# Optimization experiments

Hardware: AMD Instinct MI355X
Metric: run time of the kernel (lower is better)

Reference implementation:

```python
import jax, jax.numpy as jnp
import numpy as np

B, S, D, H = 2, 2048, 1024, 16
DK = D // H  # 64


def setup_inputs() -> dict:
    key = jax.random.key(0)
    ks = jax.random.split(key, 5)
    std = 0.02
    return {
        "x": jax.random.normal(ks[0], (B, S, D), dtype=jnp.float32),
        "Wq": jax.random.normal(ks[1], (D, D), dtype=jnp.float32) * std,
        "bq": jnp.zeros((D,), jnp.float32),
        "Wk": jax.random.normal(ks[2], (D, D), dtype=jnp.float32) * std,
        "bk": jnp.zeros((D,), jnp.float32),
        "Wv": jax.random.normal(ks[3], (D, D), dtype=jnp.float32) * std,
        "bv": jnp.zeros((D,), jnp.float32),
        "Wo": jax.random.normal(ks[4], (D, D), dtype=jnp.float32) * std,
        "bo": jnp.zeros((D,), jnp.float32),
    }


def reference(x, Wq, bq, Wk, bk, Wv, bv, Wo, bo):
    b, s, d = x.shape
    # QKV projections (torch Linear: x @ W.T + b)
    q = x @ Wq.T + bq
    k = x @ Wk.T + bk
    v = x @ Wv.T + bv
    # [b, s, d] -> [b, h, s, d_k]
    q = q.reshape(b, s, H, DK).transpose(0, 2, 1, 3)
    k = k.reshape(b, s, H, DK).transpose(0, 2, 1, 3)
    v = v.reshape(b, s, H, DK).transpose(0, 2, 1, 3)
    # scaled dot-product scores [b, h, s, s]
    scores = jnp.einsum('bhqd,bhkd->bhqk', q, k) / np.float32(np.sqrt(DK))
    # causal mask (mask=True path in original forward)
    causal = jnp.tril(jnp.ones((s, s), dtype=bool))
    scores = jnp.where(causal, scores, jnp.float32(-1e9))
    attn = jax.nn.softmax(scores, axis=-1)
    # dropout is identity in eval / p=0
    out = jnp.einsum('bhqk,bhkd->bhqd', attn, v)
    out = out.transpose(0, 2, 1, 3).reshape(b, s, d)
    return out @ Wo.T + bo
```

## Files before the change

### kernel.cpp

```cpp
#include <hip/hip_runtime.h>
#include <stdint.h>
#include <math.h>

#define B_ 2
#define S_ 2048
#define D_ 1024
#define H_ 16
#define DK_ 64
#define M_ (B_*S_)
#define NT_ 16

typedef unsigned short u16;
typedef unsigned int u32;
typedef __attribute__((ext_vector_type(8))) __bf16 bf16x8;
typedef __attribute__((ext_vector_type(4))) float f32x4;

#define AS1 __attribute__((address_space(1)))
#define AS3 __attribute__((address_space(3)))

__device__ __forceinline__ u16 f2bf(float f) {
  u32 u = __float_as_uint(f);
  return (u16)((u + 0x7fffu + ((u >> 16) & 1u)) >> 16);
}
__device__ __forceinline__ u16 f2bfr(float f) {
  return (u16)((__float_as_uint(f) + 0x8000u) >> 16);
}

__device__ __forceinline__ void gload_lds16(const void* g, void* lds) {
  __builtin_amdgcn_global_load_lds((const AS1 u32*)g,
                                   (AS3 u32*)(u32)(uintptr_t)lds, 16, 0, 0);
}

__device__ __forceinline__ f32x4 mfma16(bf16x8 a, bf16x8 b, f32x4 c) {
  return __builtin_amdgcn_mfma_f32_16x16x32_bf16(a, b, c, 0, 0, 0);
}

#define VMCNT_(n) asm volatile("s_waitcnt vmcnt(" #n ")" ::: "memory")
#define VMCNT(n) VMCNT_(n)

__global__ __launch_bounds__(256) void f2bf_kernel(const float* __restrict__ in,
                                                   u16* __restrict__ out, int n4) {
  int i = blockIdx.x * 256 + threadIdx.x;
  if (i >= n4) return;
  float4 v = ((const float4*)in)[i];
  u32 lo = (u32)f2bf(v.x) | ((u32)f2bf(v.y) << 16);
  u32 hi = (u32)f2bf(v.z) | ((u32)f2bf(v.w) << 16);
  ((uint2*)out)[i] = make_uint2(lo, hi);
}

__global__ __launch_bounds__(256) void f2bf4_kernel(
    const float* __restrict__ W0, const float* __restrict__ W1,
    const float* __restrict__ W2, const float* __restrict__ W3,
    u16* __restrict__ o0, u16* __restrict__ o1, u16* __restrict__ o2, u16* __restrict__ o3,
    int n4) {
  const float* src; u16* dst;
  switch (blockIdx.y) {
    case 0: src = W0; dst = o0; break;
    case 1: src = W1; dst = o1; break;
    case 2: src = W2; dst = o2; break;
    default: src = W3; dst = o3; break;
  }
  int i = blockIdx.x * 256 + threadIdx.x;
  if (i >= n4) return;
  float4 v = ((const float4*)src)[i];
  u32 lo = (u32)f2bf(v.x) | ((u32)f2bf(v.y) << 16);
  u32 hi = (u32)f2bf(v.z) | ((u32)f2bf(v.w) << 16);
  ((uint2*)dst)[i] = make_uint2(lo, hi);
}

__global__ __launch_bounds__(512, 2) void gemm_qkv_8ph(
    const u16* __restrict__ A,
    const u16* __restrict__ W0, const u16* __restrict__ W1, const u16* __restrict__ W2,
    const float* __restrict__ b0, const float* __restrict__ b1, const float* __restrict__ b2,
    u16* __restrict__ C0, u16* __restrict__ C1, u16* __restrict__ C2) {
  const int id = blockIdx.x;
  const int xcd = id & 7, k = id >> 3;
  const int my = xcd*2 + (k & 1);
  const int rest = k >> 1;
  const int z = rest >> 2, nx = rest & 3;

  const u16* W = (z == 0) ? W0 : (z == 1) ? W1 : W2;
  const float* bias = (z == 0) ? b0 : (z == 1) ? b1 : b2;
  u16* C = (z == 0) ? C0 : (z == 1) ? C1 : C2;
  const float osc = (z == 0) ? 0.18033688f : 1.0f;
  const int mbase = my*256, nbase = nx*256;

  __shared__ u16 LA[2][256*64];
  __shared__ u16 LB[2][256*64];

  const int tid = threadIdx.x;
  const int w = tid >> 6, lane = tid & 63;
  const int lo = lane & 15, hi = lane >> 4;
  const int wr = w >> 2, wc = w & 3;

  const int sr = tid >> 3;
  const int sc = tid & 7;
  const int sx = (sc ^ (sr & 7)) * 8;

#define STAGE_A(buf, t, h) do {                                                   \
    int gr_ = sr + (h)*64;                                                        \
    size_t g_ = (size_t)(mbase + gr_)*D_ + (size_t)(t)*64 + sx;                   \
    gload_lds16(&A[g_],            &LA[buf][gr_*64 + sc*8]);                      \
    gload_lds16(&A[g_ + 128*D_],   &LA[buf][(gr_ + 128)*64 + sc*8]);              \
  } while (0)

#define STAGE_B(buf, t, h) do {                                                   \
    int gr_ = (sr & 31) + (h)*32 + (sr >> 5)*64;                                  \
    size_t g_ = (size_t)(nbase + gr_)*D_ + (size_t)(t)*64 + sx;                   \
    gload_lds16(&W[g_],            &LB[buf][gr_*64 + sc*8]);                      \
    gload_lds16(&W[g_ + 128*D_],   &LB[buf][(gr_ + 128)*64 + sc*8]);              \
  } while (0)

#define LDA_F(dst, buf, mq, kk) do {                                              \
    _Pragma("unroll")                                                             \
    for (int m_ = 0; m_ < 4; ++m_) {                                              \
      int R_ = wr*128 + (mq)*64 + m_*16 + lo;                                     \
      dst[m_] = *(const bf16x8*)&LA[buf][R_*64 + ((((kk)*4 + hi) ^ (R_ & 7))*8)]; \
    }                                                                             \
  } while (0)

#define LDB_F(dst, buf, kk) do {                                                  \
    _Pragma("unroll")                                                             \
    for (int q_ = 0; q_ < 2; ++q_)                                                \
      _Pragma("unroll")                                                           \
      for (int n_ = 0; n_ < 2; ++n_) {                                            \
        int R_ = wc*64 + q_*32 + n_*16 + lo;                                      \
        dst[q_][n_] =                                                             \
            *(const bf16x8*)&LB[buf][R_*64 + ((((kk)*4 + hi) ^ (R_ & 7))*8)];     \
      }                                                                           \
  } while (0)

#define MM(mq, af_, bv_) do {                                                     \
    __builtin_amdgcn_s_setprio(1);                                                \
    _Pragma("unroll")                                                             \
    for (int m_ = 0; m_ < 4; ++m_)                                                \
      _Pragma("unroll")                                                           \
      for (int q_ = 0; q_ < 2; ++q_)                                              \
        _Pragma("unroll")                                                         \
        for (int n_ = 0; n_ < 2; ++n_)                                            \
          acc[(mq)*4 + m_][q_*2 + n_] =                                           \
              mfma16(bv_[q_][n_], af_[m_], acc[(mq)*4 + m_][q_*2 + n_]);          \
    __builtin_amdgcn_s_setprio(0);                                                \
  } while (0)

#define BAR __builtin_amdgcn_s_barrier()

  f32x4 acc[8][4] = {};

#define TILE(buf, t) do {                                                         \
    const int tn1_ = ((t) + 1 < NT_) ? (t) + 1 : NT_ - 1;                         \
    const int tn2_ = ((t) + 2 < NT_) ? (t) + 2 : NT_ - 1;                         \
    bf16x8 af[4], bv0[2][2], bv1[2][2];                                           \
                                                              \
    LDA_F(af, buf, 0, 0); LDB_F(bv0, buf, 0);                                     \
    STAGE_B(1 - (buf), tn1_, 1);                                                  \
    BAR; MM(0, af, bv0); BAR;                                                     \
                                                              \
    LDA_F(af, buf, 0, 1); LDB_F(bv1, buf, 1);                                     \
    STAGE_A(1 - (buf), tn1_, 1);                                                  \
    VMCNT(8);                                                                     \
    BAR; MM(0, af, bv1); BAR;                                                     \
                                                 \
    LDA_F(af, buf, 1, 0);                                                         \
    STAGE_A(buf, tn2_, 0);                                                        \
    BAR; MM(1, af, bv0); BAR;                                                     \
                                                 \
    LDA_F(af, buf, 1, 1);                                                         \
    STAGE_B(buf, tn2_, 0);                                                        \
    VMCNT(6);                                                                     \
    BAR; MM(1, af, bv1); BAR;                                                     \
  } while (0)

  STAGE_A(0, 0, 0); STAGE_B(0, 0, 0);
  STAGE_B(0, 0, 1); STAGE_A(0, 0, 1);
  STAGE_A(1, 1, 0); STAGE_B(1, 1, 0);
  VMCNT(6);
  BAR;

  for (int j = 0; j < NT_/2; ++j) {
    TILE(0, 2*j);
    TILE(1, 2*j + 1);
  }

#pragma unroll
  for (int m = 0; m < 8; ++m) {
    int row = mbase + wr*128 + m*16 + lo;
#pragma unroll
    for (int n = 0; n < 4; ++n) {
      int colb = nbase + wc*64 + n*16 + hi*4;
      float4 b4 = *(const float4*)&bias[colb];
      u32 d01 = (u32)f2bf((acc[m][n][0] + b4.x) * osc)
              | ((u32)f2bf((acc[m][n][1] + b4.y) * osc) << 16);
      u32 d23 = (u32)f2bf((acc[m][n][2] + b4.z) * osc)
              | ((u32)f2bf((acc[m][n][3] + b4.w) * osc) << 16);
      *(uint2*)&C[(size_t)row*D_ + colb] = make_uint2(d01, d23);
    }
  }
#undef TILE
#undef MM
#undef LDA_F
#undef LDB_F
#undef STAGE_A
#undef STAGE_B
#undef BAR
}

__global__ __launch_bounds__(256) void gemm_bt64(
    const u16* __restrict__ A, const u16* __restrict__ W,
    const float* __restrict__ bias, float* __restrict__ C,
    int M, int N, int K) {
  __shared__ u16 As[64*32];
  __shared__ u16 Bs[128*32];
  const int tid = threadIdx.x;
  const int wave = tid >> 6, lane = tid & 63;
  const int lo = lane & 15, hi = lane >> 4;
  const int mbase = blockIdx.y * 64, nbase = blockIdx.x * 128;

  f32x4 acc[4][2] = {};

  for (int k0 = 0; k0 < K; k0 += 32) {
    {
      int row = tid >> 2;
      int col = (tid & 3) * 8;
      gload_lds16(&A[(size_t)(mbase + row)*K + k0 + col], &As[row*32 + col]);
#pragma unroll
      for (int i = 0; i < 2; ++i)
        gload_lds16(&W[(size_t)(nbase + i*64 + row)*K + k0 + col], &Bs[(i*64 + row)*32 + col]);
    }
    __syncthreads();
    bf16x8 af[4], bfr[2];
#pragma unroll
    for (int m = 0; m < 4; ++m)
      af[m] = *(const bf16x8*)&As[(m*16 + lo)*32 + hi*8];
#pragma unroll
    for (int n = 0; n < 2; ++n)
      bfr[n] = *(const bf16x8*)&Bs[(wave*32 + n*16 + lo)*32 + hi*8];
#pragma unroll
    for (int m = 0; m < 4; ++m)
#pragma unroll
      for (int n = 0; n < 2; ++n)
        acc[m][n] = mfma16(bfr[n], af[m], acc[m][n]);
    __syncthreads();
  }

#pragma unroll
  for (int m = 0; m < 4; ++m) {
    int row = mbase + m*16 + lo;
#pragma unroll
    for (int n = 0; n < 2; ++n) {
      int colb = nbase + wave*32 + n*16 + hi*4;
      float4 b4 = *(const float4*)&bias[colb];
      float4 ov = make_float4(acc[m][n][0] + b4.x, acc[m][n][1] + b4.y,
                              acc[m][n][2] + b4.z, acc[m][n][3] + b4.w);
      *(float4*)&C[(size_t)row*N + colb] = ov;
    }
  }
}

__global__ __launch_bounds__(256) void transpose_v(const u16* __restrict__ V,
                                                   u16* __restrict__ Vt) {
  const int st = blockIdx.x, bh = blockIdx.y;
  const int b = bh >> 4, h = bh & 15;
  __shared__ u16 tile[64][72];
  const int tid = threadIdx.x;
#pragma unroll
  for (int c = 0; c < 2; ++c) {
    int s = c*32 + (tid >> 3);
    int d0 = (tid & 7) * 8;
    *(uint4*)&tile[s][d0] =
        *(const uint4*)&V[((size_t)(b*S_ + st*64 + s))*D_ + h*DK_ + d0];
  }
  __syncthreads();
#pragma unroll
  for (int c = 0; c < 2; ++c) {
    int d = c*32 + (tid >> 3);
    int s0 = (tid & 7) * 8;
    uint4 ov;
    u16* tp = (u16*)&ov;
#pragma unroll
    for (int jj = 0; jj < 8; ++jj) tp[jj] = tile[s0 + jj][d];
    *(uint4*)&Vt[((size_t)(bh*DK_ + d))*S_ + st*64 + s0] = ov;
  }
}

__global__ __launch_bounds__(256) void attn_kernel(
    const u16* __restrict__ Q, const u16* __restrict__ K, const u16* __restrict__ Vt,
    u16* __restrict__ AO) {
  const int blk = blockIdx.x;
  const int xcd = blk & 7, slot = blk >> 3;
  const int bh = xcd + 8*(slot & 3);
  const int qt = 31 - (slot >> 2);
  const int b = bh >> 4, h = bh & 15;
  const int tid = threadIdx.x, w = tid >> 6, lane = tid & 63;
  const int lo = lane & 15, hi = lane >> 4;

  __shared__ u16 Kl[2][64*64];
  __shared__ u16 Vl[2][64*64];
  __shared__ u16 Pl[4][16*72];

  const int r8 = lane >> 3;
  const int rloc = w*8 + r8;
  const int xorcol = ((lane & 7) ^ r8) * 8;
  const size_t kbase = (size_t)b*S_*D_ + (size_t)h*DK_;
  const size_t vbase = (size_t)bh*DK_*S_;
  const size_t koff0 = kbase + (size_t)rloc*D_ + xorcol;
  const size_t koff1 = kbase + (size_t)(32 + rloc)*D_ + xorcol;
  const size_t voff0 = vbase + (size_t)rloc*S_ + xorcol;
  const size_t voff1 = vbase + (size_t)(32 + rloc)*S_ + xorcol;
  const int ldsoff = rloc*64 + (lane & 7)*8;

  const int qrow = qt*64 + w*16 + lo;
  bf16x8 qf[2];
#pragma unroll
  for (int kk = 0; kk < 2; ++kk)
    qf[kk] = *(const bf16x8*)&Q[(size_t)(b*S_ + qrow)*D_ + h*DK_ + kk*32 + hi*8];

  f32x4 o[4] = {};
  float mr = -INFINITY, lr = 0.f;

  gload_lds16(&K[koff0], &Kl[0][ldsoff]);
  gload_lds16(&K[koff1], &Kl[0][2048 + ldsoff]);
  gload_lds16(&Vt[voff0], &Vl[0][ldsoff]);
  gload_lds16(&Vt[voff1], &Vl[0][2048 + ldsoff]);

  for (int kt = 0; kt <= qt; ++kt) {
    const int cur = kt & 1;
    __syncthreads();
    if (kt < qt) {
      const size_t kadd = (size_t)(kt + 1)*64*D_;
      const int vadd = (kt + 1)*64;
      gload_lds16(&K[koff0 + kadd], &Kl[cur ^ 1][ldsoff]);
      gload_lds16(&K[koff1 + kadd], &Kl[cur ^ 1][2048 + ldsoff]);
      gload_lds16(&Vt[voff0 + vadd], &Vl[cur ^ 1][ldsoff]);
      gload_lds16(&Vt[voff1 + vadd], &Vl[cur ^ 1][2048 + ldsoff]);
    }

    f32x4 s[4] = {};
#pragma unroll
    for (int kk = 0; kk < 2; ++kk) {
#pragma unroll
      for (int n = 0; n < 4; ++n) {
        int row = n*16 + lo;
        bf16x8 kf = *(const bf16x8*)&Kl[cur][row*64 + (((kk*4 + hi) ^ (row & 7)) * 8)];
        s[n] = __builtin_amdgcn_mfma_f32_16x16x32_bf16(kf, qf[kk], s[n], 0, 0, 0);
      }
    }

    if (kt == qt) {
      const int ql = w*16 + lo;
#pragma unroll
      for (int n = 0; n < 4; ++n)
#pragma unroll
        for (int j = 0; j < 4; ++j)
          if (n*16 + hi*4 + j > ql) s[n][j] = -INFINITY;
    }

    float pm = -INFINITY;
#pragma unroll
    for (int n = 0; n < 4; ++n)
#pragma unroll
      for (int j = 0; j < 4; ++j) pm = fmaxf(pm, s[n][j]);

    if (!__all(pm <= mr + 11.0f)) {
      pm = fmaxf(pm, __shfl_xor(pm, 16));
      pm = fmaxf(pm, __shfl_xor(pm, 32));
      float mn = fmaxf(mr, pm);
      float corr = __builtin_amdgcn_exp2f(mr - mn);
      mr = mn;
      lr *= corr;
#pragma unroll
      for (int n = 0; n < 4; ++n)
#pragma unroll
        for (int j = 0; j < 4; ++j) o[n][j] *= corr;
    }

#pragma unroll
    for (int n = 0; n < 4; ++n) {
      float p0 = __builtin_amdgcn_exp2f(s[n][0] - mr);
      float p1 = __builtin_amdgcn_exp2f(s[n][1] - mr);
      float p2 = __builtin_amdgcn_exp2f(s[n][2] - mr);
      float p3 = __builtin_amdgcn_exp2f(s[n][3] - mr);
      lr += (p0 + p1) + (p2 + p3);
      u32 d01 = (u32)f2bfr(p0) | ((u32)f2bfr(p1) << 16);
      u32 d23 = (u32)f2bfr(p2) | ((u32)f2bfr(p3) << 16);
      *(uint2*)&Pl[w][lo*72 + n*16 + hi*4] = make_uint2(d01, d23);
    }

#pragma unroll
    for (int kk = 0; kk < 2; ++kk) {
      bf16x8 pf = *(const bf16x8*)&Pl[w][lo*72 + kk*32 + hi*8];
#pragma unroll
      for (int n = 0; n < 4; ++n) {
        int row = n*16 + lo;
        bf16x8 vf = *(const bf16x8*)&Vl[cur][row*64 + (((kk*4 + hi) ^ (row & 7)) * 8)];
        o[n] = __builtin_amdgcn_mfma_f32_16x16x32_bf16(vf, pf, o[n], 0, 0, 0);
      }
    }
  }

  lr += __shfl_xor(lr, 16);
  lr += __shfl_xor(lr, 32);
  const float rinv = __builtin_amdgcn_rcpf(lr);
  const size_t obase = (size_t)(b*S_ + qrow)*D_ + h*DK_;
#pragma unroll
  for (int n = 0; n < 4; ++n) {
    u32 d01 = (u32)f2bf(o[n][0] * rinv) | ((u32)f2bf(o[n][1] * rinv) << 16);
    u32 d23 = (u32)f2bf(o[n][2] * rinv) | ((u32)f2bf(o[n][3] * rinv) << 16);
    *(uint2*)&AO[obase + n*16 + hi*4] = make_uint2(d01, d23);
  }
}

extern "C" void kernel_launch(void* const* d_in, const int* in_sizes, int n_in,
                              void* d_out, int out_size, void* d_ws, size_t ws_size,
                              hipStream_t stream) {
  const float* x  = (const float*)d_in[0];
  const float* Wq = (const float*)d_in[1];
  const float* bq = (const float*)d_in[2];
  const float* Wk = (const float*)d_in[3];
  const float* bk = (const float*)d_in[4];
  const float* Wv = (const float*)d_in[5];
  const float* bv = (const float*)d_in[6];
  const float* Wo = (const float*)d_in[7];
  const float* bo = (const float*)d_in[8];

  char* ws = (char*)d_ws;
  const size_t MB = 1048576;
  u16* xb  = (u16*)(ws + 0);
  u16* Wqb = (u16*)(ws + 8*MB);
  u16* Wkb = (u16*)(ws + 10*MB);
  u16* Wvb = (u16*)(ws + 12*MB);
  u16* Wob = (u16*)(ws + 14*MB);
  u16* Qb  = (u16*)(ws + 16*MB);
  u16* Kb  = (u16*)(ws + 24*MB);
  u16* Vb  = (u16*)(ws + 32*MB);
  u16* Vtb = (u16*)(ws + 0);
  u16* AOb = (u16*)(ws + 32*MB);

  f2bf_kernel<<<4096, 256, 0, stream>>>(x, xb, (M_*D_)/4);
  f2bf4_kernel<<<dim3(1024, 4), 256, 0, stream>>>(Wq, Wk, Wv, Wo,
                                                  Wqb, Wkb, Wvb, Wob, (D_*D_)/4);

  gemm_qkv_8ph<<<192, 512, 0, stream>>>(xb, Wqb, Wkb, Wvb, bq, bk, bv, Qb, Kb, Vb);

  transpose_v<<<dim3(32, 32), 256, 0, stream>>>(Vb, Vtb);

  attn_kernel<<<1024, 256, 0, stream>>>(Qb, Kb, Vtb, AOb);

  gemm_bt64<<<dim3(8, 64), 256, 0, stream>>>(AOb, Wob, bo, (float*)d_out, M_, D_, D_);
}
```

Before: 115.1 us.

## Fuse V transpose into QKV GEMM epilogue and double query rows per attention block

The QKV GEMM now swaps MFMA operand order for the V projection and writes V directly in transposed [b, feature, s] layout, which removes the separate transpose_v kernel and its round trip through global memory. The attention kernel now handles 128 query rows per block (32 per wave, in two 16-row groups), so each loaded K/V tile serves twice as many queries, and the grid is halved. Waves skip tiles that lie entirely beyond their causal limit. The cost is more registers per wave and a less balanced causal workload, and the transposed V stores are narrower and strided.

```diff
diff --git a/kernel.cpp b/kernel.cpp
--- a/kernel.cpp
+++ b/kernel.cpp
@@ -83,6 +83,7 @@
   const float* bias = (z == 0) ? b0 : (z == 1) ? b1 : b2;
   u16* C = (z == 0) ? C0 : (z == 1) ? C1 : C2;
   const float osc = (z == 0) ? 0.18033688f : 1.0f;
+  const bool vz = (z == 2);
   const int mbase = my*256, nbase = nx*256;
 
   __shared__ u16 LA[2][256*64];
@@ -132,14 +133,25 @@
 
 #define MM(mq, af_, bv_) do {                                                     \
     __builtin_amdgcn_s_setprio(1);                                                \
-    _Pragma("unroll")                                                             \
-    for (int m_ = 0; m_ < 4; ++m_)                                                \
+    if (vz) {                                                                     \
       _Pragma("unroll")                                                           \
-      for (int q_ = 0; q_ < 2; ++q_)                                              \
+      for (int m_ = 0; m_ < 4; ++m_)                                              \
         _Pragma("unroll")                                                         \
-        for (int n_ = 0; n_ < 2; ++n_)                                            \
-          acc[(mq)*4 + m_][q_*2 + n_] =                                           \
-              mfma16(bv_[q_][n_], af_[m_], acc[(mq)*4 + m_][q_*2 + n_]);          \
+        for (int q_ = 0; q_ < 2; ++q_)                                            \
+          _Pragma("unroll")                                                       \
+          for (int n_ = 0; n_ < 2; ++n_)                                          \
+            acc[(mq)*4 + m_][q_*2 + n_] =                                         \
+                mfma16(af_[m_], bv_[q_][n_], acc[(mq)*4 + m_][q_*2 + n_]);        \
+    } else {                                                                      \
+      _Pragma("unroll")                                                           \
+      for (int m_ = 0; m_ < 4; ++m_)                                              \
+        _Pragma("unroll")                                                         \
+        for (int q_ = 0; q_ < 2; ++q_)                                            \
+          _Pragma("unroll")                                                       \
+          for (int n_ = 0; n_ < 2; ++n_)                                          \
+            acc[(mq)*4 + m_][q_*2 + n_] =                                         \
+                mfma16(bv_[q_][n_], af_[m_], acc[(mq)*4 + m_][q_*2 + n_]);        \
+    }                                                                             \
     __builtin_amdgcn_s_setprio(0);                                                \
   } while (0)
 
@@ -182,18 +194,36 @@
     TILE(1, 2*j + 1);
   }
 
-#pragma unroll
-  for (int m = 0; m < 8; ++m) {
-    int row = mbase + wr*128 + m*16 + lo;
-#pragma unroll
-    for (int n = 0; n < 4; ++n) {
-      int colb = nbase + wc*64 + n*16 + hi*4;
-      float4 b4 = *(const float4*)&bias[colb];
-      u32 d01 = (u32)f2bf((acc[m][n][0] + b4.x) * osc)
-              | ((u32)f2bf((acc[m][n][1] + b4.y) * osc) << 16);
-      u32 d23 = (u32)f2bf((acc[m][n][2] + b4.z) * osc)
-              | ((u32)f2bf((acc[m][n][3] + b4.w) * osc) << 16);
-      *(uint2*)&C[(size_t)row*D_ + colb] = make_uint2(d01, d23);
+  if (!vz) {
+#pragma unroll
+    for (int m = 0; m < 8; ++m) {
+      int row = mbase + wr*128 + m*16 + lo;
+#pragma unroll
+      for (int n = 0; n < 4; ++n) {
+        int colb = nbase + wc*64 + n*16 + hi*4;
+        float4 b4 = *(const float4*)&bias[colb];
+        u32 d01 = (u32)f2bf((acc[m][n][0] + b4.x) * osc)
+                | ((u32)f2bf((acc[m][n][1] + b4.y) * osc) << 16);
+        u32 d23 = (u32)f2bf((acc[m][n][2] + b4.z) * osc)
+                | ((u32)f2bf((acc[m][n][3] + b4.w) * osc) << 16);
+        *(uint2*)&C[(size_t)row*D_ + colb] = make_uint2(d01, d23);
+      }
+    }
+  } else {
+#pragma unroll
+    for (int m = 0; m < 8; ++m) {
+      int s0 = mbase + wr*128 + m*16 + hi*4;
+      int bb = s0 >> 11, sl = s0 & (S_ - 1);
+#pragma unroll
+      for (int n = 0; n < 4; ++n) {
+        int feat = nbase + wc*64 + n*16 + lo;
+        float bvv = bias[feat];
+        u32 d01 = (u32)f2bf(acc[m][n][0] + bvv)
+                | ((u32)f2bf(acc[m][n][1] + bvv) << 16);
+        u32 d23 = (u32)f2bf(acc[m][n][2] + bvv)
+                | ((u32)f2bf(acc[m][n][3] + bvv) << 16);
+        *(uint2*)&C[((size_t)(bb*1024 + feat))*S_ + sl] = make_uint2(d01, d23);
+      }
     }
   }
 #undef TILE
@@ -257,46 +287,21 @@
   }
 }
 
-__global__ __launch_bounds__(256) void transpose_v(const u16* __restrict__ V,
-                                                   u16* __restrict__ Vt) {
-  const int st = blockIdx.x, bh = blockIdx.y;
-  const int b = bh >> 4, h = bh & 15;
-  __shared__ u16 tile[64][72];
-  const int tid = threadIdx.x;
-#pragma unroll
-  for (int c = 0; c < 2; ++c) {
-    int s = c*32 + (tid >> 3);
-    int d0 = (tid & 7) * 8;
-    *(uint4*)&tile[s][d0] =
-        *(const uint4*)&V[((size_t)(b*S_ + st*64 + s))*D_ + h*DK_ + d0];
-  }
-  __syncthreads();
-#pragma unroll
-  for (int c = 0; c < 2; ++c) {
-    int d = c*32 + (tid >> 3);
-    int s0 = (tid & 7) * 8;
-    uint4 ov;
-    u16* tp = (u16*)&ov;
-#pragma unroll
-    for (int jj = 0; jj < 8; ++jj) tp[jj] = tile[s0 + jj][d];
-    *(uint4*)&Vt[((size_t)(bh*DK_ + d))*S_ + st*64 + s0] = ov;
-  }
-}
-
 __global__ __launch_bounds__(256) void attn_kernel(
     const u16* __restrict__ Q, const u16* __restrict__ K, const u16* __restrict__ Vt,
     u16* __restrict__ AO) {
   const int blk = blockIdx.x;
   const int xcd = blk & 7, slot = blk >> 3;
   const int bh = xcd + 8*(slot & 3);
-  const int qt = 31 - (slot >> 2);
+  const int qt = 15 - (slot >> 2);
   const int b = bh >> 4, h = bh & 15;
   const int tid = threadIdx.x, w = tid >> 6, lane = tid & 63;
   const int lo = lane & 15, hi = lane >> 4;
+  const int nkt = 2*qt + 2;
 
   __shared__ u16 Kl[2][64*64];
   __shared__ u16 Vl[2][64*64];
-  __shared__ u16 Pl[4][16*72];
+  __shared__ u16 Pl[4][32*72];
 
   const int r8 = lane >> 3;
   const int rloc = w*8 + r8;
@@ -309,24 +314,30 @@
   const size_t voff1 = vbase + (size_t)(32 + rloc)*S_ + xorcol;
   const int ldsoff = rloc*64 + (lane & 7)*8;
 
-  const int qrow = qt*64 + w*16 + lo;
-  bf16x8 qf[2];
-#pragma unroll
-  for (int kk = 0; kk < 2; ++kk)
-    qf[kk] = *(const bf16x8*)&Q[(size_t)(b*S_ + qrow)*D_ + h*DK_ + kk*32 + hi*8];
-
-  f32x4 o[4] = {};
-  float mr = -INFINITY, lr = 0.f;
+  int qr[2];
+  bf16x8 qf[2][2];
+#pragma unroll
+  for (int g = 0; g < 2; ++g) {
+    qr[g] = qt*128 + w*32 + g*16 + lo;
+#pragma unroll
+    for (int kk = 0; kk < 2; ++kk)
+      qf[g][kk] = *(const bf16x8*)&Q[(size_t)(b*S_ + qr[g])*D_ + h*DK_ + kk*32 + hi*8];
+  }
+
+  f32x4 o[2][4] = {};
+  float mr[2] = {-INFINITY, -INFINITY}, lr[2] = {0.f, 0.f};
 
   gload_lds16(&K[koff0], &Kl[0][ldsoff]);
   gload_lds16(&K[koff1], &Kl[0][2048 + ldsoff]);
   gload_lds16(&Vt[voff0], &Vl[0][ldsoff]);
   gload_lds16(&Vt[voff1], &Vl[0][2048 + ldsoff]);
 
-  for (int kt = 0; kt <= qt; ++kt) {
+  const int wave_qmax = qt*128 + w*32 + 31;
+
+  for (int kt = 0; kt < nkt; ++kt) {
     const int cur = kt & 1;
     __syncthreads();
-    if (kt < qt) {
+    if (kt + 1 < nkt) {
       const size_t kadd = (size_t)(kt + 1)*64*D_;
       const int vadd = (kt + 1)*64;
       gload_lds16(&K[koff0 + kadd], &Kl[cur ^ 1][ldsoff]);
@@ -335,78 +346,94 @@
       gload_lds16(&Vt[voff1 + vadd], &Vl[cur ^ 1][2048 + ldsoff]);
     }
 
-    f32x4 s[4] = {};
+    if (kt*64 > wave_qmax) continue;
+
+    f32x4 s[2][4] = {};
 #pragma unroll
     for (int kk = 0; kk < 2; ++kk) {
 #pragma unroll
       for (int n = 0; n < 4; ++n) {
         int row = n*16 + lo;
         bf16x8 kf = *(const bf16x8*)&Kl[cur][row*64 + (((kk*4 + hi) ^ (row & 7)) * 8)];
-        s[n] = __builtin_amdgcn_mfma_f32_16x16x32_bf16(kf, qf[kk], s[n], 0, 0, 0);
-      }
-    }
-
-    if (kt == qt) {
-      const int ql = w*16 + lo;
+        s[0][n] = mfma16(kf, qf[0][kk], s[0][n]);
+        s[1][n] = mfma16(kf, qf[1][kk], s[1][n]);
+      }
+    }
+
+    if (kt >= 2*qt) {
+#pragma unroll
+      for (int g = 0; g < 2; ++g)
+#pragma unroll
+        for (int n = 0; n < 4; ++n)
+#pragma unroll
+          for (int j = 0; j < 4; ++j)
+            if (kt*64 + n*16 + hi*4 + j > qr[g]) s[g][n][j] = -INFINITY;
+    }
+
+    float pm[2] = {-INFINITY, -INFINITY};
+#pragma unroll
+    for (int g = 0; g < 2; ++g)
 #pragma unroll
       for (int n = 0; n < 4; ++n)
 #pragma unroll
-        for (int j = 0; j < 4; ++j)
-          if (n*16 + hi*4 + j > ql) s[n][j] = -INFINITY;
-    }
-
-    float pm = -INFINITY;
-#pragma unroll
-    for (int n = 0; n < 4; ++n)
-#pragma unroll
-      for (int j = 0; j < 4; ++j) pm = fmaxf(pm, s[n][j]);
-
-    if (!__all(pm <= mr + 11.0f)) {
-      pm = fmaxf(pm, __shfl_xor(pm, 16));
-      pm = fmaxf(pm, __shfl_xor(pm, 32));
-      float mn = fmaxf(mr, pm);
-      float corr = __builtin_amdgcn_exp2f(mr - mn);
-      mr = mn;
-      lr *= corr;
-#pragma unroll
-      for (int n = 0; n < 4; ++n)
-#pragma unroll
-        for (int j = 0; j < 4; ++j) o[n][j] *= corr;
-    }
-
-#pragma unroll
-    for (int n = 0; n < 4; ++n) {
-      float p0 = __builtin_amdgcn_exp2f(s[n][0] - mr);
-      float p1 = __builtin_amdgcn_exp2f(s[n][1] - mr);
-      float p2 = __builtin_amdgcn_exp2f(s[n][2] - mr);
-      float p3 = __builtin_amdgcn_exp2f(s[n][3] - mr);
-      lr += (p0 + p1) + (p2 + p3);
-      u32 d01 = (u32)f2bfr(p0) | ((u32)f2bfr(p1) << 16);
-      u32 d23 = (u32)f2bfr(p2) | ((u32)f2bfr(p3) << 16);
-      *(uint2*)&Pl[w][lo*72 + n*16 + hi*4] = make_uint2(d01, d23);
-    }
+        for (int j = 0; j < 4; ++j) pm[g] = fmaxf(pm[g], s[g][n][j]);
+
+    if (!__all(fmaxf(pm[0] - mr[0], pm[1] - mr[1]) <= 11.0f)) {
+#pragma unroll
+      for (int g = 0; g < 2; ++g) {
+        float t = fmaxf(pm[g], __shfl_xor(pm[g], 16));
+        t = fmaxf(t, __shfl_xor(t, 32));
+        float mn = fmaxf(mr[g], t);
+        float corr = __builtin_amdgcn_exp2f(mr[g] - mn);
+        mr[g] = mn;
+        lr[g] *= corr;
+#pragma unroll
+        for (int n = 0; n < 4; ++n)
+#pragma unroll
+          for (int j = 0; j < 4; ++j) o[g][n][j] *= corr;
+      }
+    }
+
+#pragma unroll
+    for (int g = 0; g < 2; ++g)
+#pragma unroll
+      for (int n = 0; n < 4; ++n) {
+        float p0 = __builtin_amdgcn_exp2f(s[g][n][0] - mr[g]);
+        float p1 = __builtin_amdgcn_exp2f(s[g][n][1] - mr[g]);
+        float p2 = __builtin_amdgcn_exp2f(s[g][n][2] - mr[g]);
+        float p3 = __builtin_amdgcn_exp2f(s[g][n][3] - mr[g]);
+        lr[g] += (p0 + p1) + (p2 + p3);
+        u32 d01 = (u32)f2bfr(p0) | ((u32)f2bfr(p1) << 16);
+        u32 d23 = (u32)f2bfr(p2) | ((u32)f2bfr(p3) << 16);
+        *(uint2*)&Pl[w][(g*16 + lo)*72 + n*16 + hi*4] = make_uint2(d01, d23);
+      }
 
 #pragma unroll
     for (int kk = 0; kk < 2; ++kk) {
-      bf16x8 pf = *(const bf16x8*)&Pl[w][lo*72 + kk*32 + hi*8];
+      bf16x8 pf0 = *(const bf16x8*)&Pl[w][lo*72 + kk*32 + hi*8];
+      bf16x8 pf1 = *(const bf16x8*)&Pl[w][(16 + lo)*72 + kk*32 + hi*8];
 #pragma unroll
       for (int n = 0; n < 4; ++n) {
         int row = n*16 + lo;
         bf16x8 vf = *(const bf16x8*)&Vl[cur][row*64 + (((kk*4 + hi) ^ (row & 7)) * 8)];
-        o[n] = __builtin_amdgcn_mfma_f32_16x16x32_bf16(vf, pf, o[n], 0, 0, 0);
-      }
-    }
-  }
-
-  lr += __shfl_xor(lr, 16);
-  lr += __shfl_xor(lr, 32);
-  const float rinv = __builtin_amdgcn_rcpf(lr);
-  const size_t obase = (size_t)(b*S_ + qrow)*D_ + h*DK_;
-#pragma unroll
-  for (int n = 0; n < 4; ++n) {
-    u32 d01 = (u32)f2bf(o[n][0] * rinv) | ((u32)f2bf(o[n][1] * rinv) << 16);
-    u32 d23 = (u32)f2bf(o[n][2] * rinv) | ((u32)f2bf(o[n][3] * rinv) << 16);
-    *(uint2*)&AO[obase + n*16 + hi*4] = make_uint2(d01, d23);
+        o[0][n] = mfma16(vf, pf0, o[0][n]);
+        o[1][n] = mfma16(vf, pf1, o[1][n]);
+      }
+    }
+  }
+
+#pragma unroll
+  for (int g = 0; g < 2; ++g) {
+    lr[g] += __shfl_xor(lr[g], 16);
+    lr[g] += __shfl_xor(lr[g], 32);
+    const float rinv = __builtin_amdgcn_rcpf(lr[g]);
+    const size_t obase = (size_t)(b*S_ + qr[g])*D_ + h*DK_;
+#pragma unroll
+    for (int n = 0; n < 4; ++n) {
+      u32 d01 = (u32)f2bf(o[g][n][0] * rinv) | ((u32)f2bf(o[g][n][1] * rinv) << 16);
+      u32 d23 = (u32)f2bf(o[g][n][2] * rinv) | ((u32)f2bf(o[g][n][3] * rinv) << 16);
+      *(uint2*)&AO[obase + n*16 + hi*4] = make_uint2(d01, d23);
+    }
   }
 }
 
@@ -432,19 +459,16 @@
   u16* Wob = (u16*)(ws + 14*MB);
   u16* Qb  = (u16*)(ws + 16*MB);
   u16* Kb  = (u16*)(ws + 24*MB);
-  u16* Vb  = (u16*)(ws + 32*MB);
-  u16* Vtb = (u16*)(ws + 0);
-  u16* AOb = (u16*)(ws + 32*MB);
+  u16* Vtb = (u16*)(ws + 32*MB);
+  u16* AOb = (u16*)(ws + 0);
 
   f2bf_kernel<<<4096, 256, 0, stream>>>(x, xb, (M_*D_)/4);
   f2bf4_kernel<<<dim3(1024, 4), 256, 0, stream>>>(Wq, Wk, Wv, Wo,
                                                   Wqb, Wkb, Wvb, Wob, (D_*D_)/4);
 
-  gemm_qkv_8ph<<<192, 512, 0, stream>>>(xb, Wqb, Wkb, Wvb, bq, bk, bv, Qb, Kb, Vb);
-
-  transpose_v<<<dim3(32, 32), 256, 0, stream>>>(Vb, Vtb);
-
-  attn_kernel<<<1024, 256, 0, stream>>>(Qb, Kb, Vtb, AOb);
+  gemm_qkv_8ph<<<192, 512, 0, stream>>>(xb, Wqb, Wkb, Wvb, bq, bk, bv, Qb, Kb, Vtb);
+
+  attn_kernel<<<512, 256, 0, stream>>>(Qb, Kb, Vtb, AOb);
 
   gemm_bt64<<<dim3(8, 64), 256, 0, stream>>>(AOb, Wob, bo, (float*)d_out, M_, D_, D_);
 }
```

Result: slower. 131.0 us (+13.9%).

## Fuse V transpose into QKV GEMM epilogue and use packed bf16 conversion

Applied to the files above, without the earlier changes.

For the V projection, the QKV GEMM swaps the MFMA operand order so each lane holds consecutive sequence positions. It then writes V directly in the transposed [b,h,d,s] layout, which removes the separate transpose_v kernel and its extra read and write of V. Bf16 packing in the GEMM epilogue and in the attention kernel now uses the hardware v_cvt_pk_bf16_f32 instruction instead of manual integer rounding. This adds a branch on the z slice inside the MFMA macro, and the transposed stores write only 8 bytes of contiguous data per lane.

```diff
diff --git a/kernel.cpp b/kernel.cpp
--- a/kernel.cpp
+++ b/kernel.cpp
@@ -22,8 +22,11 @@
   u32 u = __float_as_uint(f);
   return (u16)((u + 0x7fffu + ((u >> 16) & 1u)) >> 16);
 }
-__device__ __forceinline__ u16 f2bfr(float f) {
-  return (u16)((__float_as_uint(f) + 0x8000u) >> 16);
+
+__device__ __forceinline__ u32 cvtpk(float a, float b) {
+  u32 r;
+  asm("v_cvt_pk_bf16_f32 %0, %1, %2" : "=v"(r) : "v"(a), "v"(b));
+  return r;
 }
 
 __device__ __forceinline__ void gload_lds16(const void* g, void* lds) {
@@ -43,9 +46,8 @@
   int i = blockIdx.x * 256 + threadIdx.x;
   if (i >= n4) return;
   float4 v = ((const float4*)in)[i];
-  u32 lo = (u32)f2bf(v.x) | ((u32)f2bf(v.y) << 16);
-  u32 hi = (u32)f2bf(v.z) | ((u32)f2bf(v.w) << 16);
-  ((uint2*)out)[i] = make_uint2(lo, hi);
+  ((uint2*)out)[i] = make_uint2((u32)f2bf(v.x) | ((u32)f2bf(v.y) << 16),
+                                (u32)f2bf(v.z) | ((u32)f2bf(v.w) << 16));
 }
 
 __global__ __launch_bounds__(256) void f2bf4_kernel(
@@ -63,9 +65,8 @@
   int i = blockIdx.x * 256 + threadIdx.x;
   if (i >= n4) return;
   float4 v = ((const float4*)src)[i];
-  u32 lo = (u32)f2bf(v.x) | ((u32)f2bf(v.y) << 16);
-  u32 hi = (u32)f2bf(v.z) | ((u32)f2bf(v.w) << 16);
-  ((uint2*)dst)[i] = make_uint2(lo, hi);
+  ((uint2*)dst)[i] = make_uint2((u32)f2bf(v.x) | ((u32)f2bf(v.y) << 16),
+                                (u32)f2bf(v.z) | ((u32)f2bf(v.w) << 16));
 }
 
 __global__ __launch_bounds__(512, 2) void gemm_qkv_8ph(
@@ -83,6 +84,7 @@
   const float* bias = (z == 0) ? b0 : (z == 1) ? b1 : b2;
   u16* C = (z == 0) ? C0 : (z == 1) ? C1 : C2;
   const float osc = (z == 0) ? 0.18033688f : 1.0f;
+  const bool vz = (z == 2);
   const int mbase = my*256, nbase = nx*256;
 
   __shared__ u16 LA[2][256*64];
@@ -132,14 +134,25 @@
 
 #define MM(mq, af_, bv_) do {                                                     \
     __builtin_amdgcn_s_setprio(1);                                                \
-    _Pragma("unroll")                                                             \
-    for (int m_ = 0; m_ < 4; ++m_)                                                \
+    if (vz) {                                                                     \
       _Pragma("unroll")                                                           \
-      for (int q_ = 0; q_ < 2; ++q_)                                              \
+      for (int m_ = 0; m_ < 4; ++m_)                                              \
         _Pragma("unroll")                                                         \
-        for (int n_ = 0; n_ < 2; ++n_)                                            \
-          acc[(mq)*4 + m_][q_*2 + n_] =                                           \
-              mfma16(bv_[q_][n_], af_[m_], acc[(mq)*4 + m_][q_*2 + n_]);          \
+        for (int q_ = 0; q_ < 2; ++q_)                                            \
+          _Pragma("unroll")                                                       \
+          for (int n_ = 0; n_ < 2; ++n_)                                          \
+            acc[(mq)*4 + m_][q_*2 + n_] =                                         \
+                mfma16(af_[m_], bv_[q_][n_], acc[(mq)*4 + m_][q_*2 + n_]);        \
+    } else {                                                                      \
+      _Pragma("unroll")                                                           \
+      for (int m_ = 0; m_ < 4; ++m_)                                              \
+        _Pragma("unroll")                                                         \
+        for (int q_ = 0; q_ < 2; ++q_)                                            \
+          _Pragma("unroll")                                                       \
+          for (int n_ = 0; n_ < 2; ++n_)                                          \
+            acc[(mq)*4 + m_][q_*2 + n_] =                                         \
+                mfma16(bv_[q_][n_], af_[m_], acc[(mq)*4 + m_][q_*2 + n_]);        \
+    }                                                                             \
     __builtin_amdgcn_s_setprio(0);                                                \
   } while (0)
 
@@ -151,20 +164,16 @@
     const int tn1_ = ((t) + 1 < NT_) ? (t) + 1 : NT_ - 1;                         \
     const int tn2_ = ((t) + 2 < NT_) ? (t) + 2 : NT_ - 1;                         \
     bf16x8 af[4], bv0[2][2], bv1[2][2];                                           \
-                                                              \
     LDA_F(af, buf, 0, 0); LDB_F(bv0, buf, 0);                                     \
     STAGE_B(1 - (buf), tn1_, 1);                                                  \
     BAR; MM(0, af, bv0); BAR;                                                     \
-                                                              \
     LDA_F(af, buf, 0, 1); LDB_F(bv1, buf, 1);                                     \
     STAGE_A(1 - (buf), tn1_, 1);                                                  \
     VMCNT(8);                                                                     \
     BAR; MM(0, af, bv1); BAR;                                                     \
-                                                 \
     LDA_F(af, buf, 1, 0);                                                         \
     STAGE_A(buf, tn2_, 0);                                                        \
     BAR; MM(1, af, bv0); BAR;                                                     \
-                                                 \
     LDA_F(af, buf, 1, 1);                                                         \
     STAGE_B(buf, tn2_, 0);                                                        \
     VMCNT(6);                                                                     \
@@ -182,18 +191,32 @@
     TILE(1, 2*j + 1);
   }
 
-#pragma unroll
-  for (int m = 0; m < 8; ++m) {
-    int row = mbase + wr*128 + m*16 + lo;
-#pragma unroll
-    for (int n = 0; n < 4; ++n) {
-      int colb = nbase + wc*64 + n*16 + hi*4;
-      float4 b4 = *(const float4*)&bias[colb];
-      u32 d01 = (u32)f2bf((acc[m][n][0] + b4.x) * osc)
-              | ((u32)f2bf((acc[m][n][1] + b4.y) * osc) << 16);
-      u32 d23 = (u32)f2bf((acc[m][n][2] + b4.z) * osc)
-              | ((u32)f2bf((acc[m][n][3] + b4.w) * osc) << 16);
-      *(uint2*)&C[(size_t)row*D_ + colb] = make_uint2(d01, d23);
+  if (!vz) {
+#pragma unroll
+    for (int m = 0; m < 8; ++m) {
+      int row = mbase + wr*128 + m*16 + lo;
+#pragma unroll
+      for (int n = 0; n < 4; ++n) {
+        int colb = nbase + wc*64 + n*16 + hi*4;
+        float4 b4 = *(const float4*)&bias[colb];
+        *(uint2*)&C[(size_t)row*D_ + colb] = make_uint2(
+            cvtpk((acc[m][n][0] + b4.x) * osc, (acc[m][n][1] + b4.y) * osc),
+            cvtpk((acc[m][n][2] + b4.z) * osc, (acc[m][n][3] + b4.w) * osc));
+      }
+    }
+  } else {
+#pragma unroll
+    for (int m = 0; m < 8; ++m) {
+      int s0 = mbase + wr*128 + m*16 + hi*4;
+      int bb = s0 >> 11, sl = s0 & (S_ - 1);
+#pragma unroll
+      for (int n = 0; n < 4; ++n) {
+        int feat = nbase + wc*64 + n*16 + lo;
+        float bvv = bias[feat];
+        *(uint2*)&C[((size_t)(bb*1024 + feat))*S_ + sl] = make_uint2(
+            cvtpk(acc[m][n][0] + bvv, acc[m][n][1] + bvv),
+            cvtpk(acc[m][n][2] + bvv, acc[m][n][3] + bvv));
+      }
     }
   }
 #undef TILE
@@ -257,32 +280,6 @@
   }
 }
 
-__global__ __launch_bounds__(256) void transpose_v(const u16* __restrict__ V,
-                                                   u16* __restrict__ Vt) {
-  const int st = blockIdx.x, bh = blockIdx.y;
-  const int b = bh >> 4, h = bh & 15;
-  __shared__ u16 tile[64][72];
-  const int tid = threadIdx.x;
-#pragma unroll
-  for (int c = 0; c < 2; ++c) {
-    int s = c*32 + (tid >> 3);
-    int d0 = (tid & 7) * 8;
-    *(uint4*)&tile[s][d0] =
-        *(const uint4*)&V[((size_t)(b*S_ + st*64 + s))*D_ + h*DK_ + d0];
-  }
-  __syncthreads();
-#pragma unroll
-  for (int c = 0; c < 2; ++c) {
-    int d = c*32 + (tid >> 3);
-    int s0 = (tid & 7) * 8;
-    uint4 ov;
-    u16* tp = (u16*)&ov;
-#pragma unroll
-    for (int jj = 0; jj < 8; ++jj) tp[jj] = tile[s0 + jj][d];
-    *(uint4*)&Vt[((size_t)(bh*DK_ + d))*S_ + st*64 + s0] = ov;
-  }
-}
-
 __global__ __launch_bounds__(256) void attn_kernel(
     const u16* __restrict__ Q, const u16* __restrict__ K, const u16* __restrict__ Vt,
     u16* __restrict__ AO) {
@@ -342,7 +339,7 @@
       for (int n = 0; n < 4; ++n) {
         int row = n*16 + lo;
         bf16x8 kf = *(const bf16x8*)&Kl[cur][row*64 + (((kk*4 + hi) ^ (row & 7)) * 8)];
-        s[n] = __builtin_amdgcn_mfma_f32_16x16x32_bf16(kf, qf[kk], s[n], 0, 0, 0);
+        s[n] = mfma16(kf, qf[kk], s[n]);
       }
     }
 
@@ -381,9 +378,8 @@
       float p2 = __builtin_amdgcn_exp2f(s[n][2] - mr);
       float p3 = __builtin_amdgcn_exp2f(s[n][3] - mr);
       lr += (p0 + p1) + (p2 + p3);
-      u32 d01 = (u32)f2bfr(p0) | ((u32)f2bfr(p1) << 16);
-      u32 d23 = (u32)f2bfr(p2) | ((u32)f2bfr(p3) << 16);
-      *(uint2*)&Pl[w][lo*72 + n*16 + hi*4] = make_uint2(d01, d23);
+      *(uint2*)&Pl[w][lo*72 + n*16 + hi*4] =
+          make_uint2(cvtpk(p0, p1), cvtpk(p2, p3));
     }
 
 #pragma unroll
@@ -393,7 +389,7 @@
       for (int n = 0; n < 4; ++n) {
         int row = n*16 + lo;
         bf16x8 vf = *(const bf16x8*)&Vl[cur][row*64 + (((kk*4 + hi) ^ (row & 7)) * 8)];
-        o[n] = __builtin_amdgcn_mfma_f32_16x16x32_bf16(vf, pf, o[n], 0, 0, 0);
+        o[n] = mfma16(vf, pf, o[n]);
       }
     }
   }
@@ -404,9 +400,9 @@
   const size_t obase = (size_t)(b*S_ + qrow)*D_ + h*DK_;
 #pragma unroll
   for (int n = 0; n < 4; ++n) {
-    u32 d01 = (u32)f2bf(o[n][0] * rinv) | ((u32)f2bf(o[n][1] * rinv) << 16);
-    u32 d23 = (u32)f2bf(o[n][2] * rinv) | ((u32)f2bf(o[n][3] * rinv) << 16);
-    *(uint2*)&AO[obase + n*16 + hi*4] = make_uint2(d01, d23);
+    *(uint2*)&AO[obase + n*16 + hi*4] =
+        make_uint2(cvtpk(o[n][0] * rinv, o[n][1] * rinv),
+                   cvtpk(o[n][2] * rinv, o[n][3] * rinv));
   }
 }
 
@@ -432,17 +428,14 @@
   u16* Wob = (u16*)(ws + 14*MB);
   u16* Qb  = (u16*)(ws + 16*MB);
   u16* Kb  = (u16*)(ws + 24*MB);
-  u16* Vb  = (u16*)(ws + 32*MB);
-  u16* Vtb = (u16*)(ws + 0);
-  u16* AOb = (u16*)(ws + 32*MB);
+  u16* Vtb = (u16*)(ws + 32*MB);
+  u16* AOb = (u16*)(ws + 0);
 
   f2bf_kernel<<<4096, 256, 0, stream>>>(x, xb, (M_*D_)/4);
   f2bf4_kernel<<<dim3(1024, 4), 256, 0, stream>>>(Wq, Wk, Wv, Wo,
                                                   Wqb, Wkb, Wvb, Wob, (D_*D_)/4);
 
-  gemm_qkv_8ph<<<192, 512, 0, stream>>>(xb, Wqb, Wkb, Wvb, bq, bk, bv, Qb, Kb, Vb);
-
-  transpose_v<<<dim3(32, 32), 256, 0, stream>>>(Vb, Vtb);
+  gemm_qkv_8ph<<<192, 512, 0, stream>>>(xb, Wqb, Wkb, Wvb, bq, bk, bv, Qb, Kb, Vtb);
 
   attn_kernel<<<1024, 256, 0, stream>>>(Qb, Kb, Vtb, AOb);
 
```

Result: slower. 119.7 us (+4.0%).
